# Kernel optimization log

Measured on AMD Instinct MI355X. Metric: run time of the kernel, lower is better.

Reference implementation:

```python
import jax, jax.numpy as jnp
import numpy as np

N = 6144
D = 128
TAU = 0.1
ADJ_P = 0.005  # edge density


def _l2_normalize(x, eps=1e-12):
    # matches torch F.normalize: x / max(||x||, eps)
    n = jnp.sqrt(jnp.sum(x * x, axis=-1, keepdims=True))
    return x / jnp.maximum(n, eps)


def setup_inputs() -> dict:
    key = jax.random.key(0)
    ks = jax.random.split(key, 8)
    embF = jax.random.normal(ks[0], (N, D), jnp.float32)
    embM = jax.random.normal(ks[1], (N, D), jnp.float32)
    embP = jax.random.normal(ks[2], (N, D), jnp.float32)
    FM_adj = (jax.random.uniform(ks[3], (N, N)) < ADJ_P).astype(jnp.float32)
    FP_adj = (jax.random.uniform(ks[4], (N, N)) < ADJ_P).astype(jnp.float32)
    W1 = jax.random.normal(ks[5], (2 * D, D), jnp.float32) * (1.0 / np.sqrt(2 * D))
    b1 = jnp.zeros((D,), jnp.float32)
    W2 = jax.random.normal(ks[6], (D, 2), jnp.float32) * (1.0 / np.sqrt(D))
    b2 = jnp.zeros((2,), jnp.float32)
    return {"embF": embF, "embM": embM, "embP": embP,
            "FM_adj": FM_adj, "FP_adj": FP_adj,
            "W1": W1, "b1": b1, "W2": W2, "b2": b2}


def reference(embF, embM, embP, FM_adj, FP_adj, W1, b1, W2, b2):
    # attention-weighted neighbor aggregation
    FM_repr = (FM_adj @ embM) / jnp.maximum(FM_adj.sum(1, keepdims=True), 1.0)
    FP_repr = (FP_adj @ embP) / jnp.maximum(FP_adj.sum(1, keepdims=True), 1.0)
    # stack(dim=1).view(N,-1) == concat along feature dim
    feat = jnp.concatenate([FM_repr, FP_repr], axis=1)            # [N, 2D]
    h = jnp.maximum(feat @ W1 + b1, 0.0)                           # ReLU (dropout inactive in eval)
    weights = jax.nn.softmax(h @ W2 + b2, axis=-1)                 # [N, 2]

    Fn = _l2_normalize(embF)
    Mn = _l2_normalize(embM)
    Pn = _l2_normalize(embP)

    FM_sim = jnp.exp((Fn @ Mn.T) / TAU)                            # [N, Nm]
    FP_sim = jnp.exp((Fn @ Pn.T) / TAU)                            # [N, Np]

    FM_pos = jnp.sum(FM_sim * FM_adj, axis=1)
    FP_pos = jnp.sum(FP_sim * FP_adj, axis=1)
    FM_neg = jnp.sum(FM_sim, axis=1) - FM_pos
    FP_neg = jnp.sum(FP_sim, axis=1) - FP_pos

    w0, w1w = weights[:, 0], weights[:, 1]
    wp = w0 * FM_pos + w1w * FP_pos
    wn = w0 * FM_neg + w1w * FP_neg

    nei_count = jnp.maximum(FM_adj.sum(1) + FP_adj.sum(1), 1.0)
    ratio = wp / (wp + wn) / nei_count
    ratio = jnp.maximum(ratio, 1e-10)
    loss = jnp.mean(-jnp.log(ratio))
    return loss, weights
```

## Files before the change

### kernel.cpp

```cpp
#include <hip/hip_runtime.h>
#include <hip/hip_bf16.h>

#define NN 6144
#define DD 128
#define PBL 136
#define INV_TAU 10.0f

typedef __attribute__((ext_vector_type(4))) float f32x4;
typedef __attribute__((ext_vector_type(8))) short s16x8;

__global__ void k_normalize(const float* __restrict__ embF,
                            const float* __restrict__ embM,
                            const float* __restrict__ embP,
                            float* __restrict__ Fn,
                            float* __restrict__ rnM, float* __restrict__ rnP,
                            __hip_bfloat16* __restrict__ Fnb,
                            __hip_bfloat16* __restrict__ Mnb,
                            __hip_bfloat16* __restrict__ Pnb) {
    int which = blockIdx.y;
    const float* src = which == 0 ? embF : (which == 1 ? embM : embP);
    __hip_bfloat16* dstb = which == 0 ? Fnb : (which == 1 ? Mnb : Pnb);
    int wave = threadIdx.x >> 6, lane = threadIdx.x & 63;
    int row = blockIdx.x * 4 + wave;
    float2 v = reinterpret_cast<const float2*>(src + (size_t)row * DD)[lane];
    float s = v.x * v.x + v.y * v.y;
#pragma unroll
    for (int m = 1; m <= 32; m <<= 1) s += __shfl_xor(s, m);
    float inv = 1.0f / fmaxf(sqrtf(s), 1e-12f);
    float2 o; o.x = v.x * inv; o.y = v.y * inv;
    if (which == 0)
        reinterpret_cast<float2*>(Fn + (size_t)row * DD)[lane] = o;
    if (lane == 0) {
        if (which == 1) rnM[row] = inv;
        if (which == 2) rnP[row] = inv;
    }
    __hip_bfloat162 ob;
    ob.x = __float2bfloat16(o.x);
    ob.y = __float2bfloat16(o.y);
    reinterpret_cast<__hip_bfloat162*>(dstb + (size_t)row * DD)[lane] = ob;
}

__global__ __launch_bounds__(256) void k_sparse2(
        const float* __restrict__ FM_adj, const float* __restrict__ FP_adj,
        const float* __restrict__ embM, const float* __restrict__ embP,
        const float* __restrict__ Fn,
        const float* __restrict__ rnM, const float* __restrict__ rnP,
        float* __restrict__ feat,
        float* __restrict__ FMpos, float* __restrict__ FPpos,
        float* __restrict__ cntF, float* __restrict__ cntP) {
    __shared__ float FnS[DD];
    __shared__ int lbufT[256][4];
    __shared__ int listS[128];
    __shared__ float reprS[8][DD];
    __shared__ float posS[8];
    __shared__ int wvS[4];
    __shared__ int Ktot[2];
    const int row = blockIdx.x, h = blockIdx.y;
    const float* adj  = h ? FP_adj : FM_adj;
    const float* embX = h ? embP : embM;
    const float* RN   = h ? rnP : rnM;
    const int tid = threadIdx.x, wv = tid >> 6, lane = tid & 63;

    if (tid < 32)
        reinterpret_cast<float4*>(FnS)[tid] =
            reinterpret_cast<const float4*>(Fn + (size_t)row * DD)[tid];

    const float4* rp = reinterpret_cast<const float4*>(adj + (size_t)row * NN);
    int mycnt = 0;
#pragma unroll
    for (int it = 0; it < 6; ++it) {
        float4 v = rp[it * 256 + tid];
        int cb = (it * 256 + tid) * 4;
        if (v.x != 0.f) { if (mycnt < 4) lbufT[tid][mycnt] = cb;     mycnt++; }
        if (v.y != 0.f) { if (mycnt < 4) lbufT[tid][mycnt] = cb + 1; mycnt++; }
        if (v.z != 0.f) { if (mycnt < 4) lbufT[tid][mycnt] = cb + 2; mycnt++; }
        if (v.w != 0.f) { if (mycnt < 4) lbufT[tid][mycnt] = cb + 3; mycnt++; }
    }
    int cnt = mycnt < 4 ? mycnt : 4;
    int x = cnt;
#pragma unroll
    for (int d = 1; d < 64; d <<= 1) {
        int y = __shfl_up(x, d);
        if (lane >= d) x += y;
    }
    int t = mycnt;
#pragma unroll
    for (int msk = 1; msk <= 32; msk <<= 1) t += __shfl_xor(t, msk);
    if (tid == 0) Ktot[1] = 0;
    if (lane == 63) wvS[wv] = x;
    __syncthreads();
    if (lane == 0) atomicAdd(&Ktot[1], t);
    if (tid == 0) {
        int s = 0;
#pragma unroll
        for (int i = 0; i < 4; ++i) { int v = wvS[i]; wvS[i] = s; s += v; }
        Ktot[0] = s < 128 ? s : 128;
    }
    __syncthreads();
    int off = wvS[wv] + (x - cnt);
    for (int i = 0; i < cnt; ++i) {
        int s = off + i;
        if (s < 128) listS[s] = lbufT[tid][i];
    }
    __syncthreads();
    const int K = Ktot[0];
    const float trueK = (float)Ktot[1];

    const int hw = tid >> 5, sl = tid & 31;
    float4 f4 = reinterpret_cast<const float4*>(FnS)[sl];
    float4 racc = {0.f, 0.f, 0.f, 0.f};
    float wsum = 0.f;
    for (int k = hw; k < K; k += 8) {
        int j = listS[k];
        float rn = RN[j];
        float4 e = reinterpret_cast<const float4*>(embX + (size_t)j * DD)[sl];
        racc.x += e.x; racc.y += e.y; racc.z += e.z; racc.w += e.w;
        float d = f4.x * e.x + f4.y * e.y + f4.z * e.z + f4.w * e.w;
#pragma unroll
        for (int msk = 1; msk <= 16; msk <<= 1) d += __shfl_xor(d, msk);
        wsum += __expf(d * rn * INV_TAU);
    }
    reinterpret_cast<float4*>(&reprS[hw][0])[sl] = racc;
    if (sl == 0) posS[hw] = wsum;
    __syncthreads();
    if (tid < DD) {
        float s = 0.f;
#pragma unroll
        for (int i = 0; i < 8; ++i) s += reprS[i][tid];
        feat[(size_t)row * (2 * DD) + h * DD + tid] = s / fmaxf(trueK, 1.0f);
    }
    if (tid == 0) {
        float p = 0.f;
#pragma unroll
        for (int i = 0; i < 8; ++i) p += posS[i];
        (h ? FPpos : FMpos)[row] = p;
        (h ? cntP : cntF)[row] = trueK;
    }
}

__global__ __launch_bounds__(256) void k_dense(
        const __hip_bfloat16* __restrict__ Fnb,
        const __hip_bfloat16* __restrict__ Mnb,
        const __hip_bfloat16* __restrict__ Pnb,
        float* __restrict__ FMtot, float* __restrict__ FPtot) {
    __shared__ __hip_bfloat16 Bs[32][PBL];
    const int half = blockIdx.z;
    const __hip_bfloat16* Bnb = half ? Pnb : Mnb;
    float* TOT = half ? FPtot : FMtot;
    const int tid = threadIdx.x;
    const int w = tid >> 6, lane = tid & 63;
    const int m = lane & 15, q = lane >> 4;
    const int rb = blockIdx.x * 128 + w * 32;
    const int j0 = blockIdx.y * (NN / 16);
    const int srow = tid >> 4, scol = (tid & 15) * 8;

    s16x8 a[2][4];
#pragma unroll
    for (int g = 0; g < 2; ++g)
#pragma unroll
        for (int ks = 0; ks < 4; ++ks)
            a[g][ks] = *reinterpret_cast<const s16x8*>(
                Fnb + (size_t)(rb + g * 16 + m) * DD + ks * 32 + q * 8);

    const float4* gt0 = reinterpret_cast<const float4*>(Bnb + (size_t)j0 * DD);
    float4 s0 = gt0[tid], s1 = gt0[256 + tid];

    float tot[2][4] = {{0.f, 0.f, 0.f, 0.f}, {0.f, 0.f, 0.f, 0.f}};
    for (int it = 0; it < 12; ++it) {
        __syncthreads();
        *reinterpret_cast<float4*>(&Bs[srow][scol]) = s0;
        *reinterpret_cast<float4*>(&Bs[16 + srow][scol]) = s1;
        __syncthreads();
        if (it + 1 < 12) {
            const float4* gt = reinterpret_cast<const float4*>(
                Bnb + (size_t)(j0 + (it + 1) * 32) * DD);
            s0 = gt[tid];
            s1 = gt[256 + tid];
        }
        asm volatile("" ::: "memory");
        s16x8 b[2][4];
#pragma unroll
        for (int t = 0; t < 2; ++t)
#pragma unroll
            for (int ks = 0; ks < 4; ++ks)
                b[t][ks] = *reinterpret_cast<const s16x8*>(
                    &Bs[t * 16 + m][ks * 32 + q * 8]);
#pragma unroll
        for (int g = 0; g < 2; ++g)
#pragma unroll
            for (int t = 0; t < 2; ++t) {
                f32x4 acc = {0.f, 0.f, 0.f, 0.f};
#pragma unroll
                for (int ks = 0; ks < 4; ++ks)
                    acc = __builtin_amdgcn_mfma_f32_16x16x32_bf16(
                        a[g][ks], b[t][ks], acc, 0, 0, 0);
#pragma unroll
                for (int r = 0; r < 4; ++r)
                    tot[g][r] += __expf(acc[r] * INV_TAU);
            }
    }
#pragma unroll
    for (int msk = 1; msk <= 8; msk <<= 1)
#pragma unroll
        for (int g = 0; g < 2; ++g)
#pragma unroll
            for (int r = 0; r < 4; ++r)
                tot[g][r] += __shfl_xor(tot[g][r], msk);
    if (m == 0)
#pragma unroll
        for (int g = 0; g < 2; ++g)
#pragma unroll
            for (int r = 0; r < 4; ++r)
                atomicAdd(&TOT[rb + g * 16 + q * 4 + r], tot[g][r]);
}

__global__ __launch_bounds__(256) void k_mlp(
        const float* __restrict__ feat,
        const float* __restrict__ W1, const float* __restrict__ b1,
        const float* __restrict__ W2, const float* __restrict__ b2,
        const float* __restrict__ FMpos, const float* __restrict__ FPpos,
        const float* __restrict__ FMtot, const float* __restrict__ FPtot,
        const float* __restrict__ cntF, const float* __restrict__ cntP,
        float* __restrict__ out) {
    __shared__ float featS[8][2 * DD];
    __shared__ float partS[2][8][DD];
    __shared__ float redS[2][8][2];
    __shared__ float lossS[8];
    const int tid = threadIdx.x;
    const int cp = tid >> 7, d = tid & 127;
    const int row0 = blockIdx.x * 8;
    for (int idx = tid; idx < 8 * 2 * DD; idx += 256)
        featS[idx >> 8][idx & 255] = feat[(size_t)row0 * (2 * DD) + idx];
    __syncthreads();
    float bb = (cp == 0) ? b1[d] : 0.f;
    float acc[8];
#pragma unroll
    for (int r = 0; r < 8; ++r) acc[r] = bb;
    const int c0 = cp * 128;
    for (int c = c0; c < c0 + 128; c += 2) {
        float wA = W1[c * DD + d];
        float wB = W1[(c + 1) * DD + d];
#pragma unroll
        for (int r = 0; r < 8; ++r)
            acc[r] = fmaf(featS[r][c + 1], wB, fmaf(featS[r][c], wA, acc[r]));
    }
#pragma unroll
    for (int r = 0; r < 8; ++r) partS[cp][r][d] = acc[r];
    __syncthreads();
    if (tid < 128) {
        const int lane = tid & 63, wv = tid >> 6;
        float w20 = W2[2 * tid], w21 = W2[2 * tid + 1];
        float p0s[8], p1s[8];
#pragma unroll
        for (int r = 0; r < 8; ++r) {
            float hh = fmaxf(partS[0][r][tid] + partS[1][r][tid], 0.f);
            p0s[r] = hh * w20;
            p1s[r] = hh * w21;
        }
#pragma unroll
        for (int r = 0; r < 8; ++r)
#pragma unroll
            for (int msk = 1; msk <= 32; msk <<= 1) {
                p0s[r] += __shfl_xor(p0s[r], msk);
                p1s[r] += __shfl_xor(p1s[r], msk);
            }
        if (lane == 0)
#pragma unroll
            for (int r = 0; r < 8; ++r) {
                redS[wv][r][0] = p0s[r];
                redS[wv][r][1] = p1s[r];
            }
    }
    __syncthreads();
    if (tid < 8) {
        int row = row0 + tid;
        float z0 = redS[0][tid][0] + redS[1][tid][0] + b2[0];
        float z1 = redS[0][tid][1] + redS[1][tid][1] + b2[1];
        float mx = fmaxf(z0, z1);
        float e0 = expf(z0 - mx), e1 = expf(z1 - mx);
        float inv = 1.0f / (e0 + e1);
        float w0 = e0 * inv, w1 = e1 * inv;
        out[1 + row * 2 + 0] = w0;
        out[1 + row * 2 + 1] = w1;
        float wp = w0 * FMpos[row] + w1 * FPpos[row];
        float wn = w0 * (FMtot[row] - FMpos[row]) +
                   w1 * (FPtot[row] - FPpos[row]);
        float nei = fmaxf(cntF[row] + cntP[row], 1.0f);
        float ratio = wp / (wp + wn) / nei;
        ratio = fmaxf(ratio, 1e-10f);
        lossS[tid] = -logf(ratio);
    }
    __syncthreads();
    if (tid == 0) {
        float L = 0.f;
#pragma unroll
        for (int r = 0; r < 8; ++r) L += lossS[r];
        atomicAdd(out, L * (1.0f / NN));
    }
}

extern "C" void kernel_launch(void* const* d_in, const int* in_sizes, int n_in,
                              void* d_out, int out_size, void* d_ws, size_t ws_size,
                              hipStream_t stream) {
    const float* embF   = (const float*)d_in[0];
    const float* embM   = (const float*)d_in[1];
    const float* embP   = (const float*)d_in[2];
    const float* FM_adj = (const float*)d_in[3];
    const float* FP_adj = (const float*)d_in[4];
    const float* W1     = (const float*)d_in[5];
    const float* b1     = (const float*)d_in[6];
    const float* W2     = (const float*)d_in[7];
    const float* b2     = (const float*)d_in[8];
    float* out = (float*)d_out;

    float* ws = (float*)d_ws;
    float* FMtot = ws;
    float* FPtot = FMtot + NN;
    float* FMpos = FPtot + NN;
    float* FPpos = FMpos + NN;
    float* cntF  = FPpos + NN;
    float* cntP  = cntF + NN;
    float* rnM   = cntP + NN;
    float* rnP   = rnM + NN;
    float* feat  = rnP + NN;
    float* Fn    = feat + (size_t)NN * 2 * DD;
    __hip_bfloat16* Fnb = (__hip_bfloat16*)(Fn + (size_t)NN * DD);
    __hip_bfloat16* Mnb = Fnb + (size_t)NN * DD;
    __hip_bfloat16* Pnb = Mnb + (size_t)NN * DD;

    hipMemsetAsync(FMtot, 0, 2 * NN * sizeof(float), stream);
    hipMemsetAsync(d_out, 0, sizeof(float), stream);

    k_normalize<<<dim3(NN / 4, 3), 256, 0, stream>>>(embF, embM, embP,
                                                     Fn, rnM, rnP,
                                                     Fnb, Mnb, Pnb);
    k_sparse2<<<dim3(NN, 2), 256, 0, stream>>>(FM_adj, FP_adj, embM, embP,
                                               Fn, rnM, rnP, feat,
                                               FMpos, FPpos, cntF, cntP);
    k_dense<<<dim3(NN / 128, 16, 2), 256, 0, stream>>>(Fnb, Mnb, Pnb,
                                                       FMtot, FPtot);
    k_mlp<<<dim3(NN / 8), 256, 0, stream>>>(feat, W1, b1, W2, b2,
                                            FMpos, FPpos, FMtot, FPtot,
                                            cntF, cntP, out);
}
```

Before: 391.7 us.

## Use inline-asm async loads, double dense B tile, halve MLP rows per block

Adjacency row loads in the sparse kernel are issued as six inline-asm global_load_dwordx4 with one waitcnt, so they stay in flight together. The dense kernel stages 64 B rows per iteration instead of 32 and prefetches through asm loads, which halves the number of barriers and loop trips. The MLP kernel handles 4 rows per block instead of 8, giving twice as many blocks. Inline asm loads hide the memory dependency from the compiler, and the larger LDS tile plus extra registers may lower occupancy.

```diff
diff --git a/kernel.cpp b/kernel.cpp
--- a/kernel.cpp
+++ b/kernel.cpp
@@ -8,6 +8,13 @@
 
 typedef __attribute__((ext_vector_type(4))) float f32x4;
 typedef __attribute__((ext_vector_type(8))) short s16x8;
+
+__device__ __forceinline__ void ld4_async(const float4* p, float4& d) {
+    asm volatile("global_load_dwordx4 %0, %1, off" : "=v"(d) : "v"(p));
+}
+__device__ __forceinline__ void vm_wait0() {
+    asm volatile("s_waitcnt vmcnt(0)" ::: "memory");
+}
 
 __global__ void k_normalize(const float* __restrict__ embF,
                             const float* __restrict__ embM,
@@ -66,15 +73,23 @@
             reinterpret_cast<const float4*>(Fn + (size_t)row * DD)[tid];
 
     const float4* rp = reinterpret_cast<const float4*>(adj + (size_t)row * NN);
+    float4 v0, v1, v2, v3, v4, v5;
+    ld4_async(rp + tid,        v0);
+    ld4_async(rp + 256 + tid,  v1);
+    ld4_async(rp + 512 + tid,  v2);
+    ld4_async(rp + 768 + tid,  v3);
+    ld4_async(rp + 1024 + tid, v4);
+    ld4_async(rp + 1280 + tid, v5);
+    vm_wait0();
+    float4 vv[6] = {v0, v1, v2, v3, v4, v5};
     int mycnt = 0;
 #pragma unroll
-    for (int it = 0; it < 6; ++it) {
-        float4 v = rp[it * 256 + tid];
-        int cb = (it * 256 + tid) * 4;
-        if (v.x != 0.f) { if (mycnt < 4) lbufT[tid][mycnt] = cb;     mycnt++; }
-        if (v.y != 0.f) { if (mycnt < 4) lbufT[tid][mycnt] = cb + 1; mycnt++; }
-        if (v.z != 0.f) { if (mycnt < 4) lbufT[tid][mycnt] = cb + 2; mycnt++; }
-        if (v.w != 0.f) { if (mycnt < 4) lbufT[tid][mycnt] = cb + 3; mycnt++; }
+    for (int u = 0; u < 6; ++u) {
+        int cb = (u * 256 + tid) * 4;
+        if (vv[u].x != 0.f) { if (mycnt < 4) lbufT[tid][mycnt] = cb;     mycnt++; }
+        if (vv[u].y != 0.f) { if (mycnt < 4) lbufT[tid][mycnt] = cb + 1; mycnt++; }
+        if (vv[u].z != 0.f) { if (mycnt < 4) lbufT[tid][mycnt] = cb + 2; mycnt++; }
+        if (vv[u].w != 0.f) { if (mycnt < 4) lbufT[tid][mycnt] = cb + 3; mycnt++; }
     }
     int cnt = mycnt < 4 ? mycnt : 4;
     int x = cnt;
@@ -143,7 +158,7 @@
         const __hip_bfloat16* __restrict__ Mnb,
         const __hip_bfloat16* __restrict__ Pnb,
         float* __restrict__ FMtot, float* __restrict__ FPtot) {
-    __shared__ __hip_bfloat16 Bs[32][PBL];
+    __shared__ __hip_bfloat16 Bs[64][PBL];
     const int half = blockIdx.z;
     const __hip_bfloat16* Bnb = half ? Pnb : Mnb;
     float* TOT = half ? FPtot : FMtot;
@@ -152,7 +167,6 @@
     const int m = lane & 15, q = lane >> 4;
     const int rb = blockIdx.x * 128 + w * 32;
     const int j0 = blockIdx.y * (NN / 16);
-    const int srow = tid >> 4, scol = (tid & 15) * 8;
 
     s16x8 a[2][4];
 #pragma unroll
@@ -162,42 +176,48 @@
             a[g][ks] = *reinterpret_cast<const s16x8*>(
                 Fnb + (size_t)(rb + g * 16 + m) * DD + ks * 32 + q * 8);
 
-    const float4* gt0 = reinterpret_cast<const float4*>(Bnb + (size_t)j0 * DD);
-    float4 s0 = gt0[tid], s1 = gt0[256 + tid];
-
+    float4 s0, s1, s2, s3;
+    auto issue = [&](int jc) {
+        const float4* gp = reinterpret_cast<const float4*>(Bnb + (size_t)jc * DD);
+        ld4_async(gp + tid,       s0);
+        ld4_async(gp + 256 + tid, s1);
+        ld4_async(gp + 512 + tid, s2);
+        ld4_async(gp + 768 + tid, s3);
+    };
+    auto stash = [&](int idx, const float4& v) {
+        *reinterpret_cast<float4*>(&Bs[idx >> 4][(idx & 15) * 8]) = v;
+    };
+
+    issue(j0);
     float tot[2][4] = {{0.f, 0.f, 0.f, 0.f}, {0.f, 0.f, 0.f, 0.f}};
-    for (int it = 0; it < 12; ++it) {
+    for (int it = 0; it < 6; ++it) {
+        vm_wait0();
         __syncthreads();
-        *reinterpret_cast<float4*>(&Bs[srow][scol]) = s0;
-        *reinterpret_cast<float4*>(&Bs[16 + srow][scol]) = s1;
+        stash(tid, s0);
+        stash(256 + tid, s1);
+        stash(512 + tid, s2);
+        stash(768 + tid, s3);
         __syncthreads();
-        if (it + 1 < 12) {
-            const float4* gt = reinterpret_cast<const float4*>(
-                Bnb + (size_t)(j0 + (it + 1) * 32) * DD);
-            s0 = gt[tid];
-            s1 = gt[256 + tid];
-        }
-        asm volatile("" ::: "memory");
-        s16x8 b[2][4];
-#pragma unroll
-        for (int t = 0; t < 2; ++t)
+        if (it + 1 < 6) issue(j0 + (it + 1) * 64);
+#pragma unroll
+        for (int t = 0; t < 4; ++t) {
+            s16x8 b[4];
 #pragma unroll
             for (int ks = 0; ks < 4; ++ks)
-                b[t][ks] = *reinterpret_cast<const s16x8*>(
+                b[ks] = *reinterpret_cast<const s16x8*>(
                     &Bs[t * 16 + m][ks * 32 + q * 8]);
 #pragma unroll
-        for (int g = 0; g < 2; ++g)
-#pragma unroll
-            for (int t = 0; t < 2; ++t) {
+            for (int g = 0; g < 2; ++g) {
                 f32x4 acc = {0.f, 0.f, 0.f, 0.f};
 #pragma unroll
                 for (int ks = 0; ks < 4; ++ks)
                     acc = __builtin_amdgcn_mfma_f32_16x16x32_bf16(
-                        a[g][ks], b[t][ks], acc, 0, 0, 0);
+                        a[g][ks], b[ks], acc, 0, 0, 0);
 #pragma unroll
                 for (int r = 0; r < 4; ++r)
                     tot[g][r] += __expf(acc[r] * INV_TAU);
             }
+        }
     }
 #pragma unroll
     for (int msk = 1; msk <= 8; msk <<= 1)
@@ -222,43 +242,43 @@
         const float* __restrict__ FMtot, const float* __restrict__ FPtot,
         const float* __restrict__ cntF, const float* __restrict__ cntP,
         float* __restrict__ out) {
-    __shared__ float featS[8][2 * DD];
-    __shared__ float partS[2][8][DD];
-    __shared__ float redS[2][8][2];
-    __shared__ float lossS[8];
+    __shared__ float featS[4][2 * DD];
+    __shared__ float partS[2][4][DD];
+    __shared__ float redS[2][4][2];
+    __shared__ float lossS[4];
     const int tid = threadIdx.x;
     const int cp = tid >> 7, d = tid & 127;
-    const int row0 = blockIdx.x * 8;
-    for (int idx = tid; idx < 8 * 2 * DD; idx += 256)
+    const int row0 = blockIdx.x * 4;
+    for (int idx = tid; idx < 4 * 2 * DD; idx += 256)
         featS[idx >> 8][idx & 255] = feat[(size_t)row0 * (2 * DD) + idx];
     __syncthreads();
     float bb = (cp == 0) ? b1[d] : 0.f;
-    float acc[8];
-#pragma unroll
-    for (int r = 0; r < 8; ++r) acc[r] = bb;
+    float acc[4];
+#pragma unroll
+    for (int r = 0; r < 4; ++r) acc[r] = bb;
     const int c0 = cp * 128;
     for (int c = c0; c < c0 + 128; c += 2) {
         float wA = W1[c * DD + d];
         float wB = W1[(c + 1) * DD + d];
 #pragma unroll
-        for (int r = 0; r < 8; ++r)
+        for (int r = 0; r < 4; ++r)
             acc[r] = fmaf(featS[r][c + 1], wB, fmaf(featS[r][c], wA, acc[r]));
     }
 #pragma unroll
-    for (int r = 0; r < 8; ++r) partS[cp][r][d] = acc[r];
+    for (int r = 0; r < 4; ++r) partS[cp][r][d] = acc[r];
     __syncthreads();
     if (tid < 128) {
         const int lane = tid & 63, wv = tid >> 6;
         float w20 = W2[2 * tid], w21 = W2[2 * tid + 1];
-        float p0s[8], p1s[8];
-#pragma unroll
-        for (int r = 0; r < 8; ++r) {
+        float p0s[4], p1s[4];
+#pragma unroll
+        for (int r = 0; r < 4; ++r) {
             float hh = fmaxf(partS[0][r][tid] + partS[1][r][tid], 0.f);
             p0s[r] = hh * w20;
             p1s[r] = hh * w21;
         }
 #pragma unroll
-        for (int r = 0; r < 8; ++r)
+        for (int r = 0; r < 4; ++r)
 #pragma unroll
             for (int msk = 1; msk <= 32; msk <<= 1) {
                 p0s[r] += __shfl_xor(p0s[r], msk);
@@ -266,13 +286,13 @@
             }
         if (lane == 0)
 #pragma unroll
-            for (int r = 0; r < 8; ++r) {
+            for (int r = 0; r < 4; ++r) {
                 redS[wv][r][0] = p0s[r];
                 redS[wv][r][1] = p1s[r];
             }
     }
     __syncthreads();
-    if (tid < 8) {
+    if (tid < 4) {
         int row = row0 + tid;
         float z0 = redS[0][tid][0] + redS[1][tid][0] + b2[0];
         float z1 = redS[0][tid][1] + redS[1][tid][1] + b2[1];
@@ -294,7 +314,7 @@
     if (tid == 0) {
         float L = 0.f;
 #pragma unroll
-        for (int r = 0; r < 8; ++r) L += lossS[r];
+        for (int r = 0; r < 4; ++r) L += lossS[r];
         atomicAdd(out, L * (1.0f / NN));
     }
 }
@@ -339,7 +359,7 @@
                                                FMpos, FPpos, cntF, cntP);
     k_dense<<<dim3(NN / 128, 16, 2), 256, 0, stream>>>(Fnb, Mnb, Pnb,
                                                        FMtot, FPtot);
-    k_mlp<<<dim3(NN / 8), 256, 0, stream>>>(feat, W1, b1, W2, b2,
+    k_mlp<<<dim3(NN / 4), 256, 0, stream>>>(feat, W1, b1, W2, b2,
                                             FMpos, FPpos, FMtot, FPtot,
                                             cntF, cntP, out);
 }
```

After: 395.0 us. No clear change (+0.8%).
